# Kernel optimization log

Hardware: AMD Instinct MI355X
Metric: run time of the kernel (lower is better)

The kernel has to match this reference:

```python
import jax, jax.numpy as jnp
import numpy as np

B, T, D = 1, 2048, 4096
N_HEADS, KV_HEADS, HEAD_DIM = 32, 8, 128
WINDOW = 1024
ROPE_THETA = 500000.0
EPS = 1e-6
LARGE_NEGATIVE = np.finfo(np.float32).min


def _rms_norm(x, w, eps=EPS):
    xf = x.astype(jnp.float32)
    out = xf * jax.lax.rsqrt(jnp.square(xf).mean(-1, keepdims=True) + eps)
    return (w.astype(jnp.float32) * out).astype(x.dtype)


def _positions_from_segment_ids(seg_ids):
    t = seg_ids.shape[1]
    return jax.vmap(lambda row: jnp.where(row != 0, jnp.arange(t) - jnp.argmax(row), 2 ** 30))(seg_ids)


def _rope_sin_cos(positions, head_dim=HEAD_DIM, theta=ROPE_THETA):
    fraction = jnp.arange(0, head_dim, 2, dtype=jnp.float32) / head_dim
    inv_freq = 1.0 / (theta ** fraction)
    sinusoid = jnp.einsum('BT,k->BTk', positions.astype(jnp.float32), inv_freq)
    return jnp.sin(sinusoid), jnp.cos(sinusoid)


def _apply_rope(x, sin, cos):
    half = x.shape[-1] // 2
    x1, x2 = x[..., :half], x[..., half:]
    sin, cos = sin[:, :, None, :], cos[:, :, None, :]
    return jnp.concatenate([x1 * cos - x2 * sin, x2 * cos + x1 * sin], axis=-1).astype(x.dtype)


def setup_inputs() -> dict:
    key = jax.random.key(0)
    ks = jax.random.split(key, 6)
    wscale = 1.0 / np.sqrt(D)
    return {
        'x': jax.random.normal(ks[0], (B, T, D), dtype=jnp.float32),
        'Wq': jax.random.normal(ks[1], (D, N_HEADS * HEAD_DIM), dtype=jnp.float32) * wscale,
        'Wk': jax.random.normal(ks[2], (D, KV_HEADS * HEAD_DIM), dtype=jnp.float32) * wscale,
        'Wv': jax.random.normal(ks[3], (D, KV_HEADS * HEAD_DIM), dtype=jnp.float32) * wscale,
        'Wo': jax.random.normal(ks[4], (N_HEADS * HEAD_DIM, D), dtype=jnp.float32) * wscale,
        'q_norm_w': jnp.ones((N_HEADS * HEAD_DIM,), dtype=jnp.float32),
        'k_norm_w': jnp.ones((KV_HEADS * HEAD_DIM,), dtype=jnp.float32),
        'segment_ids': jnp.ones((B, T), dtype=jnp.int32),
    }


def reference(x, Wq, Wk, Wv, Wo, q_norm_w, k_norm_w, segment_ids):
    b, t, _ = x.shape
    positions = _positions_from_segment_ids(segment_ids)
    sin, cos = _rope_sin_cos(positions)

    # QKV projections; q/k RMS-normed over the flattened (heads*head_dim) axis pre-reshape.
    q = _rms_norm(x @ Wq, q_norm_w).reshape(b, t, N_HEADS, HEAD_DIM)
    k = _rms_norm(x @ Wk, k_norm_w).reshape(b, t, KV_HEADS, HEAD_DIM)
    v = (x @ Wv).reshape(b, t, KV_HEADS, HEAD_DIM)

    q = _apply_rope(q, sin, cos)
    k = _apply_rope(k, sin, cos)

    # GQA: physically repeat kv heads (repeat_kv in source).
    n_rep = N_HEADS // KV_HEADS
    k = jnp.repeat(k[:, :, :, None, :], n_rep, axis=3).reshape(b, t, N_HEADS, HEAD_DIM)
    v = jnp.repeat(v[:, :, :, None, :], n_rep, axis=3).reshape(b, t, N_HEADS, HEAD_DIM)

    # causal + sliding-window + same-segment mask, [B, T, S]
    i = positions[:, :, None]
    j = positions[:, None, :]
    same_seg = segment_ids[:, :, None] == segment_ids[:, None, :]
    mask = (j <= i) & ((i - j) < WINDOW) & same_seg & (segment_ids != 0)[:, None, :]

    scale = HEAD_DIM ** -0.5
    logits = jnp.einsum('BTNH,BSNH->BNTS', q, k) * jnp.array(scale, dtype=q.dtype)
    padded = jnp.where(mask[:, None, :, :], logits.astype(jnp.float32), LARGE_NEGATIVE)
    probs = jax.nn.softmax(padded, axis=-1).astype(k.dtype)
    attn = jnp.einsum('BNTS,BSNH->BTNH', probs, v)
    return attn.reshape(b, t, N_HEADS * HEAD_DIM) @ Wo
```

## Files before the change

### kernel.cpp

```cpp
#include <hip/hip_runtime.h>
#include <cstdint>
#include <cstddef>

typedef __bf16 bf16_t;
typedef __bf16 bf16x8 __attribute__((ext_vector_type(8)));
typedef __bf16 bf16x4 __attribute__((ext_vector_type(4)));
typedef __bf16 bf16x2 __attribute__((ext_vector_type(2)));
typedef float f32x4 __attribute__((ext_vector_type(4)));

#define T_LEN 2048
#define DMODEL 4096
#define NHEADS 32
#define KVHEADS 8
#define HD 128
#define QD 4096
#define KD 1024
#define QKVD 6144
#define WIN 1024
#define VS 72

__global__ void pos_kernel(const int* __restrict__ seg, int* __restrict__ positions) {
  __shared__ int svals[256], sidx[256];
  int tid = threadIdx.x;
  int bestv = -2147483647 - 1, besti = 0;
  for (int t = tid; t < T_LEN; t += 256) {
    int v = seg[t];
    if (v > bestv) { bestv = v; besti = t; }
  }
  svals[tid] = bestv; sidx[tid] = besti;
  __syncthreads();
  for (int st = 128; st > 0; st >>= 1) {
    if (tid < st) {
      if (svals[tid+st] > svals[tid] || (svals[tid+st] == svals[tid] && sidx[tid+st] < sidx[tid])) {
        svals[tid] = svals[tid+st]; sidx[tid] = sidx[tid+st];
      }
    }
    __syncthreads();
  }
  int amax = sidx[0];
  for (int t = tid; t < T_LEN; t += 256)
    positions[t] = (seg[t] != 0) ? (t - amax) : (1 << 30);
}

__global__ void sincos_kernel(const int* __restrict__ positions, float* __restrict__ sc) {
  int t = blockIdx.x, i = threadIdx.x;
  float inv = expf(-(float)i * (logf(500000.0f) / 64.0f));
  float ang = (float)positions[t] * inv;
  sc[(t*64 + i)*2 + 0] = sinf(ang);
  sc[(t*64 + i)*2 + 1] = cosf(ang);
}

__global__ void cvt_kernel(const float* __restrict__ in, bf16_t* __restrict__ out, int n) {
  int i = (blockIdx.x * blockDim.x + threadIdx.x) * 8;
  if (i >= n) return;
  float4 a = *(const float4*)(in + i);
  float4 b = *(const float4*)(in + i + 4);
  bf16x8 o;
  o[0]=(bf16_t)a.x; o[1]=(bf16_t)a.y; o[2]=(bf16_t)a.z; o[3]=(bf16_t)a.w;
  o[4]=(bf16_t)b.x; o[5]=(bf16_t)b.y; o[6]=(bf16_t)b.z; o[7]=(bf16_t)b.w;
  *(bf16x8*)(out + i) = o;
}

__global__ void transcvt_kernel(const float* __restrict__ W, bf16_t* __restrict__ Wt, int K, int N) {
  __shared__ float tile[32][33];
  int tx = threadIdx.x, ty = threadIdx.y;
  int bx = blockIdx.x, by = blockIdx.y;
  #pragma unroll
  for (int i = 0; i < 4; i++) {
    int k = by*32 + ty + i*8;
    tile[ty + i*8][tx] = W[(size_t)k * N + bx*32 + tx];
  }
  __syncthreads();
  int t = ty*32 + tx;
  int n = t >> 3;
  int kq = t & 7;
  bf16x4 v;
  #pragma unroll
  for (int e = 0; e < 4; e++) v[e] = (bf16_t)tile[kq*4 + e][n];
  *(bf16x4*)(Wt + (size_t)(bx*32 + n) * K + by*32 + kq*4) = v;
}

__device__ __forceinline__ void gld_lds16(const void* g, void* l) {
  __builtin_amdgcn_global_load_lds((__attribute__((address_space(1))) void*)g,
                                   (__attribute__((address_space(3))) void*)l, 16, 0, 0);
}

#define MFMA_QUAD(FM0, FN0)                                                     \
  { _Pragma("unroll") for (int fm_ = 0; fm_ < QFM; fm_++)                        \
    _Pragma("unroll") for (int fn_ = 0; fn_ < 2; fn_++)                          \
    _Pragma("unroll") for (int kk_ = 0; kk_ < 2; kk_++)                          \
      acc[(FM0)+fm_][(FN0)+fn_] = __builtin_amdgcn_mfma_f32_16x16x32_bf16(       \
          a[(FM0)+fm_][kk_], bb[(FN0)+fn_][kk_], acc[(FM0)+fm_][(FN0)+fn_], 0,0,0); }

template<bool WRITE_BF16, int AM>
__global__ __launch_bounds__(512, 2) void gemm256_kernel(
    const bf16_t* __restrict__ A, const bf16_t* __restrict__ Bt,
    bf16_t* __restrict__ Cb, float* __restrict__ Cf,
    int M, int N, int K, int NBM) {
  constexpr int BM  = AM * 128;
  constexpr int NH  = AM + 2;
  constexpr int FM2 = AM * 4;
  constexpr int QFM = AM * 2;
  __shared__ bf16_t As[2 * BM * 64];
  __shared__ bf16_t Bs[2 * 256 * 64];
  int tid = threadIdx.x;
  int w = tid >> 6, l = tid & 63, lr = l & 15, lg = l >> 4;
  int wr = w >> 2, wc = w & 3;
  int nwg = gridDim.x;
  int wg  = blockIdx.x;
  int cpx = nwg >> 3;
  int swz = (wg & 7) * cpx + (wg >> 3);
  int bm = swz % NBM, bn = swz / NBM;
  const int NT = K >> 6;

  auto stage = [&](int tt, int h) {
    int b2 = tt & 1;
    const bf16_t* G; size_t grow0; bf16_t* ldsb;
    if (h < AM) { G = A;  grow0 = (size_t)bm*BM + h*128;        ldsb = As + b2*(BM*64) + h*8192; }
    else        { G = Bt; grow0 = (size_t)bn*256 + (h-AM)*128;  ldsb = Bs + b2*16384 + (h-AM)*8192; }
    int kcol = tt * 64;
    #pragma unroll
    for (int r2 = 0; r2 < 2; r2++) {
      int L = r2*8192 + tid*16;
      int row = L >> 7;
      int chunk = (L >> 4) & 7;
      int scn = chunk ^ (row & 7);
      gld_lds16(G + (grow0 + (size_t)row) * K + kcol + scn*8,
                ldsb + r2*4096 + w*512);
    }
  };
  auto afrag = [&](int b2, int row, int kk) -> bf16x8 {
    int chunk = (kk*4 + lg) ^ (row & 7);
    return *(const bf16x8*)((const char*)(As + b2*(BM*64)) + row*128 + chunk*16);
  };
  auto bfrag = [&](int b2, int row, int kk) -> bf16x8 {
    int chunk = (kk*4 + lg) ^ (row & 7);
    return *(const bf16x8*)((const char*)(Bs + b2*16384) + row*128 + chunk*16);
  };

  f32x4 acc[FM2][4] = {};
  bf16x8 a[FM2][2], bb[4][2];

  #pragma unroll
  for (int h = 0; h < NH; h++) stage(0, h);
  #pragma unroll
  for (int h = 0; h < NH - 1; h++) stage(1, h);
  if constexpr (AM == 2) asm volatile("s_waitcnt vmcnt(6)" ::: "memory");
  else                   asm volatile("s_waitcnt vmcnt(4)" ::: "memory");
  __builtin_amdgcn_s_barrier();

  for (int t = 0; t < NT; t++) {
    int b = t & 1;
    #pragma unroll
    for (int fm = 0; fm < FM2; fm++)
      #pragma unroll
      for (int kk = 0; kk < 2; kk++)
        a[fm][kk] = afrag(b, wr*(BM/2) + fm*16 + lr, kk);
    #pragma unroll
    for (int fn = 0; fn < 2; fn++)
      #pragma unroll
      for (int kk = 0; kk < 2; kk++)
        bb[fn][kk] = bfrag(b, wc*64 + fn*16 + lr, kk);
    if (t + 1 < NT) stage(t + 1, NH - 1);
    __builtin_amdgcn_s_barrier();
    asm volatile("s_waitcnt lgkmcnt(0)" ::: "memory");
    __builtin_amdgcn_s_setprio(1);
    MFMA_QUAD(0, 0);
    __builtin_amdgcn_s_setprio(0);
    __builtin_amdgcn_s_barrier();
    #pragma unroll
    for (int fn = 2; fn < 4; fn++)
      #pragma unroll
      for (int kk = 0; kk < 2; kk++)
        bb[fn][kk] = bfrag(b, wc*64 + fn*16 + lr, kk);
    if (t + 2 < NT) stage(t + 2, 0);
    __builtin_amdgcn_s_barrier();
    asm volatile("s_waitcnt lgkmcnt(0)" ::: "memory");
    __builtin_amdgcn_s_setprio(1);
    MFMA_QUAD(0, 2);
    __builtin_amdgcn_s_setprio(0);
    __builtin_amdgcn_s_barrier();
    if (t + 2 < NT) stage(t + 2, 1);
    __builtin_amdgcn_s_barrier();
    __builtin_amdgcn_s_setprio(1);
    MFMA_QUAD(QFM, 2);
    __builtin_amdgcn_s_setprio(0);
    __builtin_amdgcn_s_barrier();
    if constexpr (AM == 2) { if (t + 2 < NT) stage(t + 2, 2); }
    __builtin_amdgcn_s_barrier();
    __builtin_amdgcn_s_setprio(1);
    MFMA_QUAD(QFM, 0);
    __builtin_amdgcn_s_setprio(0);
    if (t < NT - 2) {
      if constexpr (AM == 2) asm volatile("s_waitcnt vmcnt(6)" ::: "memory");
      else                   asm volatile("s_waitcnt vmcnt(4)" ::: "memory");
    } else {
      asm volatile("s_waitcnt vmcnt(0)" ::: "memory");
    }
    __builtin_amdgcn_s_barrier();
  }

  #pragma unroll
  for (int fm = 0; fm < FM2; fm++) {
    #pragma unroll
    for (int fn = 0; fn < 4; fn++) {
      #pragma unroll
      for (int r2 = 0; r2 < 4; r2++) {
        int row = bm*BM + wr*(BM/2) + fm*16 + lg*4 + r2;
        int col = bn*256 + wc*64 + fn*16 + lr;
        if (WRITE_BF16) Cb[(size_t)row * N + col] = (bf16_t)acc[fm][fn][r2];
        else            Cf[(size_t)row * N + col] = acc[fm][fn][r2];
      }
    }
  }
}

__global__ __launch_bounds__(256) void normrope_kernel(bf16_t* __restrict__ qkv,
    const float* __restrict__ qw, const float* __restrict__ kw,
    const float* __restrict__ sc) {
  int t = blockIdx.x;
  int tid = threadIdx.x;
  bf16_t* qrow = qkv + (size_t)t * QKVD;
  bf16_t* krow = qrow + QD;
  __shared__ float red[8];
  float s = 0.f;
  {
    const bf16x8* p = (const bf16x8*)(qrow + tid*16);
    bf16x8 v0 = p[0], v1 = p[1];
    #pragma unroll
    for (int j = 0; j < 8; j++) { float a = (float)v0[j], b = (float)v1[j]; s += a*a + b*b; }
  }
  #pragma unroll
  for (int o = 32; o; o >>= 1) s += __shfl_xor(s, o);
  if ((tid & 63) == 0) red[tid >> 6] = s;
  float sk = 0.f;
  {
    bf16x4 v = *(const bf16x4*)(krow + tid*4);
    #pragma unroll
    for (int j = 0; j < 4; j++) { float a = (float)v[j]; sk += a*a; }
  }
  #pragma unroll
  for (int o = 32; o; o >>= 1) sk += __shfl_xor(sk, o);
  if ((tid & 63) == 0) red[4 + (tid >> 6)] = sk;
  __syncthreads();
  float rq = rsqrtf((red[0]+red[1]+red[2]+red[3]) / (float)QD + 1e-6f);
  float rk = rsqrtf((red[4]+red[5]+red[6]+red[7]) / (float)KD + 1e-6f);
  const float ascale = 0.08838834764831845f;
  for (int p = tid; p < 2048; p += 256) {
    int hh = p >> 6, i = p & 63;
    int i1 = hh*HD + i, i2 = i1 + 64;
    float x1 = (float)qrow[i1] * rq * qw[i1];
    float x2 = (float)qrow[i2] * rq * qw[i2];
    float sn = sc[(t*64 + i)*2 + 0], cs = sc[(t*64 + i)*2 + 1];
    qrow[i1] = (bf16_t)((x1*cs - x2*sn) * ascale);
    qrow[i2] = (bf16_t)((x2*cs + x1*sn) * ascale);
  }
  for (int p = tid; p < 512; p += 256) {
    int hh = p >> 6, i = p & 63;
    int i1 = hh*HD + i, i2 = i1 + 64;
    float x1 = (float)krow[i1] * rk * kw[i1];
    float x2 = (float)krow[i2] * rk * kw[i2];
    float sn = sc[(t*64 + i)*2 + 0], cs = sc[(t*64 + i)*2 + 1];
    krow[i1] = (bf16_t)(x1*cs - x2*sn);
    krow[i2] = (bf16_t)(x2*cs + x1*sn);
  }
}

__global__ __launch_bounds__(512, 3) void attn_kernel(const bf16_t* __restrict__ qkv,
    const int* __restrict__ positions, const int* __restrict__ seg,
    bf16_t* __restrict__ O) {
  __shared__ bf16_t Ks[64 * HD];
  __shared__ bf16_t Vt[HD * VS];
  __shared__ bf16_t P[8][16 * VS];
  int tid = threadIdx.x;
  int w = tid >> 6, l = tid & 63, lr = l & 15, lg = l >> 4;
  int qb = blockIdx.x * 128;
  int h = blockIdx.y;
  int kvh = h >> 2;
  int q0 = qb + w * 16;
  const bf16_t* Kg = qkv + QD + (size_t)kvh * HD;
  const bf16_t* Vg = qkv + QD + KD + (size_t)kvh * HD;

  bf16x8 qf[4];
  {
    const bf16_t* Qrow = qkv + (size_t)(q0 + lr) * QKVD + h * HD;
    #pragma unroll
    for (int c = 0; c < 4; c++) qf[c] = *(const bf16x8*)(Qrow + c*32 + lg*8);
  }
  int pos_i[4], seg_i[4];
  #pragma unroll
  for (int r = 0; r < 4; r++) { int i = q0 + lg*4 + r; pos_i[r] = positions[i]; seg_i[r] = seg[i]; }
  f32x4 o[8] = {};
  float m[4], lsum[4];
  #pragma unroll
  for (int r = 0; r < 4; r++) { m[r] = -__builtin_inff(); lsum[r] = 0.f; }

  int vkp = tid & 31, vdg = tid >> 5;
  bf16x8 vrA, vrB;

  auto issueK = [&](int j0) {
    #pragma unroll
    for (int i = 0; i < 2; i++) {
      int c = tid + i*512;
      int row = c >> 4;
      int scn = (c & 15) ^ (row & 7);
      gld_lds16(Kg + (size_t)(j0 + row) * QKVD + scn*8,
                (char*)Ks + (size_t)(i*512 + (tid & 448))*16);
    }
  };
  auto loadV = [&](int j0) {
    const bf16_t* vp = Vg + (size_t)(j0 + 2*vkp) * QKVD + vdg*8;
    vrA = *(const bf16x8*)vp;
    vrB = *(const bf16x8*)(vp + QKVD);
  };

  int jstart = qb - (WIN - 1); if (jstart < 0) jstart = 0; jstart &= ~63;
  const int jlast = qb + 64;
  loadV(jstart);
  issueK(jstart);

  for (int j0 = jstart; j0 <= jlast; j0 += 64) {
    #pragma unroll
    for (int e = 0; e < 8; e++) {
      bf16x2 pr; pr[0] = vrA[e]; pr[1] = vrB[e];
      *(bf16x2*)(Vt + (vdg*8 + e)*VS + 2*vkp) = pr;
    }
    int pj[4], sj[4];
    #pragma unroll
    for (int kt = 0; kt < 4; kt++) { int j = j0 + kt*16 + lr; pj[kt] = positions[j]; sj[kt] = seg[j]; }
    asm volatile("" ::: "memory");
    if (j0 + 64 <= jlast) loadV(j0 + 64);
    asm volatile("" ::: "memory");
    asm volatile("s_waitcnt vmcnt(2) lgkmcnt(0)" ::: "memory");
    __builtin_amdgcn_s_barrier();

    bool active = (j0 <= q0 + 15) && (j0 + 63 >= q0 - (WIN - 1));
    if (active) {
      f32x4 s[4] = {};
      __builtin_amdgcn_s_setprio(1);
      #pragma unroll
      for (int kt = 0; kt < 4; kt++) {
        int row = kt*16 + lr;
        const char* kb = (const char*)Ks + row*256;
        #pragma unroll
        for (int c = 0; c < 4; c++) {
          bf16x8 kf = *(const bf16x8*)(kb + (((c*4 + lg) ^ (row & 7)) * 16));
          s[kt] = __builtin_amdgcn_mfma_f32_16x16x32_bf16(qf[c], kf, s[kt], 0, 0, 0);
        }
      }
      __builtin_amdgcn_s_setprio(0);
      #pragma unroll
      for (int kt = 0; kt < 4; kt++) {
        #pragma unroll
        for (int r = 0; r < 4; r++) {
          bool valid = (pj[kt] <= pos_i[r]) && (pos_i[r] - pj[kt] < WIN) && (seg_i[r] == sj[kt]) && (sj[kt] != 0);
          s[kt][r] = valid ? s[kt][r] : -__builtin_inff();
        }
      }
      #pragma unroll
      for (int r = 0; r < 4; r++) {
        float smax = fmaxf(fmaxf(s[0][r], s[1][r]), fmaxf(s[2][r], s[3][r]));
        if (__any(smax > m[r] + 8.f)) {
          float rm = smax;
          #pragma unroll
          for (int o2 = 1; o2 < 16; o2 <<= 1) rm = fmaxf(rm, __shfl_xor(rm, o2));
          if (rm > m[r] + 8.f) {
            float rescale = __expf(m[r] - rm);
            lsum[r] *= rescale;
            #pragma unroll
            for (int n = 0; n < 8; n++) o[n][r] *= rescale;
            m[r] = rm;
          }
        }
        float mub = fmaxf(m[r], -1e37f);
        float p0 = __expf(s[0][r] - mub);
        float p1 = __expf(s[1][r] - mub);
        float p2 = __expf(s[2][r] - mub);
        float p3 = __expf(s[3][r] - mub);
        lsum[r] += (p0 + p1) + (p2 + p3);
        int prow = (lg*4 + r) * VS;
        P[w][prow + lr]      = (bf16_t)p0;
        P[w][prow + 16 + lr] = (bf16_t)p1;
        P[w][prow + 32 + lr] = (bf16_t)p2;
        P[w][prow + 48 + lr] = (bf16_t)p3;
      }
    }
    __builtin_amdgcn_s_barrier();
    asm volatile("" ::: "memory");

    if (j0 + 64 <= jlast) issueK(j0 + 64);
    if (active) {
      __builtin_amdgcn_s_setprio(1);
      #pragma unroll
      for (int ks = 0; ks < 2; ks++) {
        bf16x8 pa = *(const bf16x8*)(&P[w][lr*VS + ks*32 + lg*8]);
        #pragma unroll
        for (int n = 0; n < 8; n++) {
          bf16x8 vb = *(const bf16x8*)(&Vt[(n*16 + lr)*VS + ks*32 + lg*8]);
          o[n] = __builtin_amdgcn_mfma_f32_16x16x32_bf16(pa, vb, o[n], 0, 0, 0);
        }
      }
      __builtin_amdgcn_s_setprio(0);
    }
    __builtin_amdgcn_s_barrier();
  }
  #pragma unroll
  for (int r = 0; r < 4; r++) {
    float ls = lsum[r];
    #pragma unroll
    for (int o2 = 1; o2 < 16; o2 <<= 1) ls += __shfl_xor(ls, o2);
    float inv = ls > 0.f ? 1.f / ls : 0.f;
    int row = q0 + lg*4 + r;
    #pragma unroll
    for (int n = 0; n < 8; n++)
      O[(size_t)row * QD + h*HD + n*16 + lr] = (bf16_t)(o[n][r] * inv);
  }
}

extern "C" void kernel_launch(void* const* d_in, const int* in_sizes, int n_in,
                              void* d_out, int out_size, void* d_ws, size_t ws_size,
                              hipStream_t stream) {
  (void)in_sizes; (void)n_in; (void)out_size; (void)ws_size;
  const float* x  = (const float*)d_in[0];
  const float* Wq = (const float*)d_in[1];
  const float* Wk = (const float*)d_in[2];
  const float* Wv = (const float*)d_in[3];
  const float* Wo = (const float*)d_in[4];
  const float* qw = (const float*)d_in[5];
  const float* kw = (const float*)d_in[6];
  const int*  seg = (const int*)d_in[7];
  float* out = (float*)d_out;

  char* base = (char*)d_ws;
  size_t off = 0;
  auto alloc = [&](size_t b) { void* r = base + off; off = (off + b + 255) & ~(size_t)255; return r; };
  bf16_t* xb    = (bf16_t*)alloc((size_t)T_LEN * DMODEL * 2);
  bf16_t* Wallt = (bf16_t*)alloc((size_t)QKVD * DMODEL * 2);
  bf16_t* Wot   = (bf16_t*)alloc((size_t)DMODEL * QD * 2);
  bf16_t* qkv   = (bf16_t*)alloc((size_t)T_LEN * QKVD * 2);
  int*    posi  = (int*)alloc((size_t)T_LEN * 4);
  float*  sc    = (float*)alloc((size_t)T_LEN * 64 * 2 * 4);
  bf16_t* ao    = xb;

  pos_kernel<<<1, 256, 0, stream>>>(seg, posi);
  sincos_kernel<<<T_LEN, 64, 0, stream>>>(posi, sc);
  cvt_kernel<<<(T_LEN * DMODEL / 8 + 255) / 256, 256, 0, stream>>>(x, xb, T_LEN * DMODEL);
  transcvt_kernel<<<dim3(QD/32, DMODEL/32), dim3(32, 8), 0, stream>>>(Wq, Wallt, DMODEL, QD);
  transcvt_kernel<<<dim3(KD/32, DMODEL/32), dim3(32, 8), 0, stream>>>(Wk, Wallt + (size_t)QD * DMODEL, DMODEL, KD);
  transcvt_kernel<<<dim3(KD/32, DMODEL/32), dim3(32, 8), 0, stream>>>(Wv, Wallt + (size_t)(QD + KD) * DMODEL, DMODEL, KD);
  transcvt_kernel<<<dim3(DMODEL/32, QD/32), dim3(32, 8), 0, stream>>>(Wo, Wot, QD, DMODEL);
  gemm256_kernel<true, 2><<<dim3((T_LEN/256)*(QKVD/256)), 512, 0, stream>>>(
      xb, Wallt, qkv, nullptr, T_LEN, QKVD, DMODEL, T_LEN/256);
  normrope_kernel<<<T_LEN, 256, 0, stream>>>(qkv, qw, kw, sc);
  attn_kernel<<<dim3(T_LEN/128, NHEADS), 512, 0, stream>>>(qkv, posi, seg, ao);
  gemm256_kernel<false, 1><<<dim3((T_LEN/128)*(DMODEL/256)), 512, 0, stream>>>(
      ao, Wot, nullptr, out, T_LEN, DMODEL, QD, T_LEN/128);
}
```

Before: 375.6 us.

## Add 256x192-tile QKV GEMM kernel to improve CU occupancy balance

Adds a dedicated GEMM kernel for the fused QKV projection that uses 256x192 output tiles instead of 256x256. The grid grows from 192 to 256 workgroups, which matches the MI355X CU count more closely and reduces the partial tail wave. Inside the loop it uses a staged schedule that interleaves LDS fragment loads, global-to-LDS prefetch and MFMA groups under barriers. The cost is smaller per-tile reuse and a hand-scheduled pipeline whose wait counts must stay correct.

```diff
diff --git a/kernel.cpp b/kernel.cpp
--- a/kernel.cpp
+++ b/kernel.cpp
@@ -83,6 +83,138 @@
 __device__ __forceinline__ void gld_lds16(const void* g, void* l) {
   __builtin_amdgcn_global_load_lds((__attribute__((address_space(1))) void*)g,
                                    (__attribute__((address_space(3))) void*)l, 16, 0, 0);
+}
+
+__global__ __launch_bounds__(512, 2) void gemm192_kernel(
+    const bf16_t* __restrict__ A, const bf16_t* __restrict__ Bt,
+    bf16_t* __restrict__ Cb, int M, int N, int K, int NBM) {
+  __shared__ bf16_t As[2 * 256 * 64];
+  __shared__ bf16_t Bs[2 * 192 * 64];
+  int tid = threadIdx.x;
+  int w = tid >> 6, l = tid & 63, lr = l & 15, lg = l >> 4;
+  int wr = w >> 2, wc = w & 3;
+  int nwg = gridDim.x;
+  int wg  = blockIdx.x;
+  int cpx = nwg >> 3;
+  int swz = (wg & 7) * cpx + (wg >> 3);
+  int bm = swz % NBM, bn = swz / NBM;
+  const int NT = K >> 6;
+
+  auto stageA = [&](int tt, int h) {
+    int b2 = tt & 1;
+    bf16_t* ldsb = As + b2*16384 + h*8192;
+    #pragma unroll
+    for (int r2 = 0; r2 < 2; r2++) {
+      int L = r2*8192 + tid*16;
+      int row = L >> 7;
+      int chunk = (L >> 4) & 7;
+      int scn = chunk ^ (row & 7);
+      gld_lds16(A + ((size_t)bm*256 + h*128 + row) * K + tt*64 + scn*8,
+                ldsb + r2*4096 + w*512);
+    }
+  };
+  auto stageB = [&](int tt, int u) {
+    int b2 = tt & 1;
+    bf16_t* ldsb = Bs + b2*12288 + u*4096;
+    int row = tid >> 3;
+    int scn = (tid & 7) ^ (row & 7);
+    gld_lds16(Bt + ((size_t)bn*192 + u*64 + row) * K + tt*64 + scn*8,
+              ldsb + w*512);
+  };
+  auto afrag = [&](int b2, int row, int kk) -> bf16x8 {
+    int chunk = (kk*4 + lg) ^ (row & 7);
+    return *(const bf16x8*)((const char*)(As + b2*16384) + row*128 + chunk*16);
+  };
+  auto bfrag = [&](int b2, int row, int kk) -> bf16x8 {
+    int chunk = (kk*4 + lg) ^ (row & 7);
+    return *(const bf16x8*)((const char*)(Bs + b2*12288) + row*128 + chunk*16);
+  };
+
+  f32x4 acc[8][3] = {};
+  bf16x8 a[8][2], bb[3][2];
+
+  stageA(0, 0); stageA(0, 1); stageB(0, 0); stageB(0, 1); stageB(0, 2);
+  stageA(1, 0); stageA(1, 1); stageB(1, 0); stageB(1, 1);
+  asm volatile("s_waitcnt vmcnt(6)" ::: "memory");
+  __builtin_amdgcn_s_barrier();
+
+  for (int t = 0; t < NT; t++) {
+    int b = t & 1;
+    #pragma unroll
+    for (int fm = 0; fm < 8; fm++)
+      #pragma unroll
+      for (int kk = 0; kk < 2; kk++)
+        a[fm][kk] = afrag(b, wr*128 + fm*16 + lr, kk);
+    #pragma unroll
+    for (int fn = 0; fn < 2; fn++)
+      #pragma unroll
+      for (int kk = 0; kk < 2; kk++)
+        bb[fn][kk] = bfrag(b, wc*48 + fn*16 + lr, kk);
+    if (t + 1 < NT) stageB(t + 1, 2);
+    __builtin_amdgcn_s_barrier();
+    asm volatile("s_waitcnt lgkmcnt(0)" ::: "memory");
+    __builtin_amdgcn_s_setprio(1);
+    #pragma unroll
+    for (int fm = 0; fm < 4; fm++)
+      #pragma unroll
+      for (int fn = 0; fn < 2; fn++)
+        #pragma unroll
+        for (int kk = 0; kk < 2; kk++)
+          acc[fm][fn] = __builtin_amdgcn_mfma_f32_16x16x32_bf16(a[fm][kk], bb[fn][kk], acc[fm][fn], 0, 0, 0);
+    __builtin_amdgcn_s_setprio(0);
+    __builtin_amdgcn_s_barrier();
+    #pragma unroll
+    for (int kk = 0; kk < 2; kk++)
+      bb[2][kk] = bfrag(b, wc*48 + 32 + lr, kk);
+    if (t + 2 < NT) stageA(t + 2, 0);
+    __builtin_amdgcn_s_barrier();
+    asm volatile("s_waitcnt lgkmcnt(0)" ::: "memory");
+    __builtin_amdgcn_s_setprio(1);
+    #pragma unroll
+    for (int fm = 0; fm < 4; fm++)
+      #pragma unroll
+      for (int kk = 0; kk < 2; kk++)
+        acc[fm][2] = __builtin_amdgcn_mfma_f32_16x16x32_bf16(a[fm][kk], bb[2][kk], acc[fm][2], 0, 0, 0);
+    __builtin_amdgcn_s_setprio(0);
+    __builtin_amdgcn_s_barrier();
+    if (t + 2 < NT) stageA(t + 2, 1);
+    __builtin_amdgcn_s_barrier();
+    __builtin_amdgcn_s_setprio(1);
+    #pragma unroll
+    for (int fm = 4; fm < 8; fm++)
+      #pragma unroll
+      for (int kk = 0; kk < 2; kk++)
+        acc[fm][2] = __builtin_amdgcn_mfma_f32_16x16x32_bf16(a[fm][kk], bb[2][kk], acc[fm][2], 0, 0, 0);
+    __builtin_amdgcn_s_setprio(0);
+    __builtin_amdgcn_s_barrier();
+    if (t + 2 < NT) { stageB(t + 2, 0); stageB(t + 2, 1); }
+    __builtin_amdgcn_s_barrier();
+    __builtin_amdgcn_s_setprio(1);
+    #pragma unroll
+    for (int fm = 4; fm < 8; fm++)
+      #pragma unroll
+      for (int fn = 0; fn < 2; fn++)
+        #pragma unroll
+        for (int kk = 0; kk < 2; kk++)
+          acc[fm][fn] = __builtin_amdgcn_mfma_f32_16x16x32_bf16(a[fm][kk], bb[fn][kk], acc[fm][fn], 0, 0, 0);
+    __builtin_amdgcn_s_setprio(0);
+    if (t < NT - 2) asm volatile("s_waitcnt vmcnt(6)" ::: "memory");
+    else            asm volatile("s_waitcnt vmcnt(0)" ::: "memory");
+    __builtin_amdgcn_s_barrier();
+  }
+
+  #pragma unroll
+  for (int fm = 0; fm < 8; fm++) {
+    #pragma unroll
+    for (int fn = 0; fn < 3; fn++) {
+      #pragma unroll
+      for (int r2 = 0; r2 < 4; r2++) {
+        int row = bm*256 + wr*128 + fm*16 + lg*4 + r2;
+        int col = bn*192 + wc*48 + fn*16 + lr;
+        Cb[(size_t)row * N + col] = (bf16_t)acc[fm][fn][r2];
+      }
+    }
+  }
 }
 
 #define MFMA_QUAD(FM0, FN0)                                                     \
@@ -449,8 +581,8 @@
   transcvt_kernel<<<dim3(KD/32, DMODEL/32), dim3(32, 8), 0, stream>>>(Wk, Wallt + (size_t)QD * DMODEL, DMODEL, KD);
   transcvt_kernel<<<dim3(KD/32, DMODEL/32), dim3(32, 8), 0, stream>>>(Wv, Wallt + (size_t)(QD + KD) * DMODEL, DMODEL, KD);
   transcvt_kernel<<<dim3(DMODEL/32, QD/32), dim3(32, 8), 0, stream>>>(Wo, Wot, QD, DMODEL);
-  gemm256_kernel<true, 2><<<dim3((T_LEN/256)*(QKVD/256)), 512, 0, stream>>>(
-      xb, Wallt, qkv, nullptr, T_LEN, QKVD, DMODEL, T_LEN/256);
+  gemm192_kernel<<<dim3((T_LEN/256)*(QKVD/192)), 512, 0, stream>>>(
+      xb, Wallt, qkv, T_LEN, QKVD, DMODEL, T_LEN/256);
   normrope_kernel<<<T_LEN, 256, 0, stream>>>(qkv, qw, kw, sc);
   attn_kernel<<<dim3(T_LEN/128, NHEADS), 512, 0, stream>>>(qkv, posi, seg, ao);
   gemm256_kernel<false, 1><<<dim3((T_LEN/128)*(DMODEL/256)), 512, 0, stream>>>(
```

New measurement: 360.9 us. 1.04x faster.
